# Performance work log

Measured on AMD Instinct MI355X. Metric: run time of the kernel, lower is better.

The kernel has to match this reference:

```python
import jax, jax.numpy as jnp
import numpy as np

# static config (matches init_kwargs)
C = 64            # dim_split = dim // 4
DIM = 256
HID = 128         # int(dim//4 * mlp_ratio), mlp_ratio=2
S = 64            # state_dim
NH, HD = 16, 4    # GA: num_heads = C // head_dim, head_dim = 4
AK, AP = 11, 5    # att_kernel, att_padding
B, H, W = 8, 28, 28


def conv2d(x, w, pad, stride=1, groups=1, bias=None):
    out = jax.lax.conv_general_dilated(
        x, w, (stride, stride), pad, feature_group_count=groups,
        dimension_numbers=('NCHW', 'OIHW', 'NCHW'))
    if bias is not None:
        out = out + bias[None, :, None, None]
    return out


def pw(x, w, b=None):  # 1x1 conv, w: (O, Cin)
    y = jnp.einsum('oc,bchw->bohw', w, x)
    return y if b is None else y + b[None, :, None, None]


def bn(x, p, eps=1e-5):  # eval-mode BatchNorm2d; p: (4, C) = gamma, beta, mean, var
    g, b, m, v = p
    s = g / jnp.sqrt(v + eps)
    return (x - m[None, :, None, None]) * s[None, :, None, None] + b[None, :, None, None]


def relu6(x):
    return jnp.minimum(jax.nn.relu(x), 6.0)


def maxpool3(x):  # 3x3, stride 1, pad 1
    return jax.lax.reduce_window(x, -jnp.inf, jax.lax.max, (1, 1, 3, 3), (1, 1, 1, 1),
                                 [(0, 0), (0, 0), (1, 1), (1, 1)])


def blurpool(x):  # antialiased_cnns.BlurPool(channels, stride=3), filt_size=4
    a = np.array([1.0, 3.0, 3.0, 1.0])
    filt = np.outer(a, a)
    filt = filt / filt.sum()
    c = x.shape[1]
    w = jnp.asarray(np.tile(filt[None, None], (c, 1, 1, 1)), x.dtype)
    xp = jnp.pad(x, ((0, 0), (0, 0), (1, 2), (1, 2)), mode='reflect')
    return conv2d(xp, w, [(0, 0), (0, 0)], stride=3, groups=c)


def h_transform(x):
    b, c, hs, ws = x.shape
    x = jnp.pad(x, ((0, 0), (0, 0), (0, 0), (0, ws))).reshape(b, c, -1)[..., :-ws]
    return x.reshape(b, c, hs, 2 * ws - 1)


def inv_h_transform(x):
    b, c, hs, _ = x.shape
    x = jnp.pad(x.reshape(b, c, -1), ((0, 0), (0, 0), (0, hs)))
    return x.reshape(b, c, hs, 2 * hs)[..., :hs]


def v_transform(x):
    return h_transform(x.transpose(0, 1, 3, 2)).transpose(0, 1, 3, 2)


def inv_v_transform(x):
    return inv_h_transform(x.transpose(0, 1, 3, 2)).transpose(0, 1, 3, 2)


def _forward(x, dw1_w, dw1_b, bn_dw1, f1_w, f1_b, f2_w, f2_b, g_w, g_b, bn_g,
             dw2_w, dw2_b, hatt1_w, vatt1_w, hatt2_w, vatt2_w, bn_mra,
             bcdt_w, ssd_dw_w, hz_w, out_w, A_param, D_param,
             qkv_w, proj_w, bn_norm4, mlp1_w, bn_mlp, mlp2_w, bn_norm1):
    shortcut = x
    x1, x2, x3, x4 = jnp.split(x, 4, axis=1)

    # --- branch 1: dwconv + star-gated MLP ---
    x1o = bn(conv2d(x1, dw1_w, [(3, 3), (3, 3)], groups=C, bias=dw1_b), bn_dw1)
    x1 = relu6(pw(x1o, f1_w, f1_b)) * pw(x1o, f2_w, f2_b)
    x1 = conv2d(bn(pw(x1, g_w, g_b), bn_g), dw2_w, [(3, 3), (3, 3)], groups=C, bias=dw2_b)

    # --- branch 2: MRA ---
    xt = blurpool(maxpool3(x2))  # (B, C, 10, 10)
    xh1 = conv2d(xt, hatt1_w, [(AP, AP), (1, 1)], groups=C)
    xw1 = conv2d(xt, vatt1_w, [(1, 1), (AP, AP)], groups=C)
    xh2 = inv_h_transform(conv2d(h_transform(xt), hatt2_w, [(AP, AP), (1, 1)], groups=C))
    xw2 = inv_v_transform(conv2d(v_transform(xt), vatt2_w, [(1, 1), (AP, AP)], groups=C))
    att = jax.nn.sigmoid(bn(xh1 + xw1 + xh2 + xw2, bn_mra))
    hs, ws = att.shape[-2], att.shape[-1]
    ri = (jnp.arange(H) * hs) // H  # nearest-neighbor upsampling indices
    ci = (jnp.arange(W) * ws) // W
    x2 = x2 * att[:, :, ri][:, :, :, ci]

    # --- branch 3: HSMSSD (hidden-state-mixer SSD) ---
    L = H * W
    xs = x3.reshape(B, C, L)
    bcdt = conv2d(jnp.einsum('oc,bcl->bol', bcdt_w, xs).reshape(B, 3 * S, H, W),
                  ssd_dw_w, [(1, 1), (1, 1)], groups=3 * S).reshape(B, 3 * S, L)
    Bm, Cm, dt = jnp.split(bcdt, 3, axis=1)              # each (B, S, L)
    A = jax.nn.softmax(dt + A_param[None, :, None], axis=-1)
    h = jnp.einsum('bcl,bsl->bcs', xs, A * Bm)           # (B, C, S)
    h_, z = jnp.split(jnp.einsum('oc,bcs->bos', hz_w, h), 2, axis=1)
    h_ = jnp.einsum('oc,bcs->bos', out_w, h_ * jax.nn.silu(z) + h_ * D_param)
    x3 = jnp.einsum('bcs,bsl->bcl', h_, Cm).reshape(B, C, H, W)

    # --- branch 4: GA full attention + BN residual (stage == 3) ---
    t = x4.reshape(B, C, L).transpose(0, 2, 1)           # (B, N, C)
    qkv = (t @ qkv_w.T).reshape(B, L, 3, NH, HD).transpose(2, 0, 3, 1, 4)
    q, k, v = qkv[0], qkv[1], qkv[2]
    attn = jax.nn.softmax(jnp.einsum('bhnd,bhmd->bhnm', q, k) * HD ** -0.5, axis=-1)
    o = jnp.einsum('bhnm,bhmd->bhnd', attn, v).transpose(0, 2, 1, 3).reshape(B, L, NH * HD)
    x4 = bn(x4 + (o @ proj_w.T).transpose(0, 2, 1).reshape(B, C, H, W), bn_norm4)

    # --- merge + MLP ---
    xa = jnp.concatenate([x1, x2, x3, x4], axis=1)
    m = pw(jax.nn.relu(bn(pw(xa, mlp1_w), bn_mlp)), mlp2_w)
    return shortcut + bn(m, bn_norm1)


def setup_inputs() -> dict:
    key = jax.random.key(0)
    ks = iter(jax.random.split(key, 64))

    def w(shape, s=0.05):
        return jax.random.normal(next(ks), shape, dtype=jnp.float32) * s

    def bnp(c):
        g = 1.0 + 0.1 * jax.random.normal(next(ks), (c,), dtype=jnp.float32)
        b = 0.1 * jax.random.normal(next(ks), (c,), dtype=jnp.float32)
        m = 0.1 * jax.random.normal(next(ks), (c,), dtype=jnp.float32)
        v = 0.5 + jax.random.uniform(next(ks), (c,), dtype=jnp.float32)
        return jnp.stack([g, b, m, v])

    return dict(
        x=jax.random.normal(next(ks), (B, DIM, H, W), dtype=jnp.float32),
        dw1_w=w((C, 1, 7, 7), 0.1), dw1_b=w((C,), 0.02), bn_dw1=bnp(C),
        f1_w=w((HID, C)), f1_b=w((HID,), 0.02),
        f2_w=w((HID, C)), f2_b=w((HID,), 0.02),
        g_w=w((C, HID)), g_b=w((C,), 0.02), bn_g=bnp(C),
        dw2_w=w((C, 1, 7, 7), 0.1), dw2_b=w((C,), 0.02),
        hatt1_w=w((C, 1, AK, 3), 0.1), vatt1_w=w((C, 1, 3, AK), 0.1),
        hatt2_w=w((C, 1, AK, 3), 0.1), vatt2_w=w((C, 1, 3, AK), 0.1),
        bn_mra=bnp(C),
        bcdt_w=w((3 * S, C)), ssd_dw_w=w((3 * S, 1, 3, 3), 0.1),
        hz_w=w((2 * C, C)), out_w=w((C, C)),
        A_param=jax.random.uniform(next(ks), (S,), dtype=jnp.float32, minval=1.0, maxval=16.0),
        D_param=jnp.ones((1,), dtype=jnp.float32),
        qkv_w=w((3 * NH * HD, C)), proj_w=w((C, NH * HD)),
        bn_norm4=bnp(C),
        mlp1_w=w((HID, DIM)), bn_mlp=bnp(HID), mlp2_w=w((DIM, HID)),
        bn_norm1=bnp(DIM),
    )


def reference(x, dw1_w, dw1_b, bn_dw1, f1_w, f1_b, f2_w, f2_b, g_w, g_b, bn_g,
              dw2_w, dw2_b, hatt1_w, vatt1_w, hatt2_w, vatt2_w, bn_mra,
              bcdt_w, ssd_dw_w, hz_w, out_w, A_param, D_param,
              qkv_w, proj_w, bn_norm4, mlp1_w, bn_mlp, mlp2_w, bn_norm1):
    return _forward(x, dw1_w, dw1_b, bn_dw1, f1_w, f1_b, f2_w, f2_b, g_w, g_b, bn_g,
                    dw2_w, dw2_b, hatt1_w, vatt1_w, hatt2_w, vatt2_w, bn_mra,
                    bcdt_w, ssd_dw_w, hz_w, out_w, A_param, D_param,
                    qkv_w, proj_w, bn_norm4, mlp1_w, bn_mlp, mlp2_w, bn_norm1)
```

## Files before the change

kernel.cpp:

```cpp
#include <hip/hip_runtime.h>
#include <hip/hip_bf16.h>
#include <math.h>

#define DEV __device__ __forceinline__

constexpr int B=8, C=64, DIM=256, HID=128, S=64, NH=16, HD=4, LPIX=784;
constexpr int NPIX = B*LPIX;
constexpr int CH   = (NPIX+255)/256;
constexpr int QB   = 12*((NPIX+511)/512);

constexpr size_t OFF_X1O = 0;
constexpr size_t OFF_T1  = OFF_X1O + (size_t)B*C*LPIX;
constexpr size_t OFF_T2  = OFF_T1  + (size_t)B*HID*LPIX;
constexpr size_t OFF_XA  = OFF_T2  + (size_t)B*C*LPIX;
constexpr size_t OFF_BC2 = OFF_XA  + (size_t)B*DIM*LPIX;
constexpr size_t OFF_WGT = OFF_BC2 + (size_t)B*192*LPIX;
constexpr size_t OFF_H   = OFF_WGT + (size_t)B*S*LPIX;
constexpr size_t OFF_HO  = OFF_H   + (size_t)4*B*C*S;
constexpr size_t OFF_QKV = OFF_HO  + (size_t)B*C*S;
constexpr size_t OFF_O   = OFF_QKV + (size_t)3*B*NH*LPIX*HD;
constexpr size_t OFF_LS  = OFF_O   + (size_t)4*B*LPIX*C;
constexpr size_t OFF_MID = OFF_LS  + (size_t)4*B*NH*LPIX;

DEV float bnorm(float x, const float* p, int c, int nc){
  float g=p[c], bb=p[nc+c], m=p[2*nc+c], v=p[3*nc+c];
  return (x-m)*(g*rsqrtf(v+1e-5f))+bb;
}
DEV int refl(int p){ int k=p-1; if(k<0)k=-k; if(k>27)k=54-k; return k; }

DEV bool upix(int blk, int tid, int ngroups, int& grp, int& b, int& l){
  grp = blk % ngroups;
  int gidx = (blk/ngroups)*256 + tid;
  if(gidx >= NPIX) return false;
  b = gidx / LPIX; l = gidx % LPIX;
  return true;
}

DEV void body_dw1t(int bc, int tid, float* xs, const float* X, const float* w, const float* bias, const float* bnp, float* out){
  int c = bc & 63, b = bc >> 6;
  const float* xp = X + ((size_t)(b*DIM+c))*LPIX;
  for(int i=tid;i<34*34;i+=256) xs[i]=0.f;
  __syncthreads();
  for(int i=tid;i<LPIX;i+=256){ int y=i/28, x=i%28; xs[(y+3)*34+(x+3)]=xp[i]; }
  __syncthreads();
  const float* wc = w + (size_t)c*49;
  float bs = bias[c];
  for(int i=tid;i<LPIX;i+=256){
    int y=i/28, x=i%28;
    float s = bs;
    #pragma unroll
    for(int ky=0;ky<7;ky++){
      #pragma unroll
      for(int kx=0;kx<7;kx++)
        s += xs[(y+ky)*34 + x+kx]*wc[ky*7+kx];
    }
    out[((size_t)(b*C+c))*LPIX + i] = bnorm(s,bnp,c,C);
  }
}

DEV void body_branch2(int bc, int tid, float* smem, const float* X,
                      const float* h1w,const float* v1w,const float* h2w,const float* v2w,
                      const float* bnp, float* xa){
  int c = bc & 63, b = bc >> 6;
  float* xs  = smem;
  float* mp  = smem+LPIX;
  float* xt  = smem+2*LPIX;
  float* attv= smem+2*LPIX+100;
  const float* xp = X + ((size_t)(b*DIM+64+c))*LPIX;
  for(int i=tid;i<LPIX;i+=256) xs[i]=xp[i];
  __syncthreads();
  for(int i=tid;i<LPIX;i+=256){
    int y=i/28, x=i%28;
    float m=-1e30f;
    for(int dy=-1;dy<=1;dy++){ int iy=y+dy; if(iy<0||iy>=28) continue;
      for(int dx=-1;dx<=1;dx++){ int ix=x+dx; if(ix<0||ix>=28) continue;
        m=fmaxf(m,xs[iy*28+ix]); } }
    mp[i]=m;
  }
  __syncthreads();
  if(tid<100){
    int ii=tid/10, j=tid%10;
    const float fw[4]={0.125f,0.375f,0.375f,0.125f};
    float s=0;
    for(int ky=0;ky<4;ky++){ int rr=refl(3*ii+ky);
      for(int kx=0;kx<4;kx++){ int cc=refl(3*j+kx);
        s += fw[ky]*fw[kx]*mp[rr*28+cc]; } }
    xt[tid]=s;
  }
  __syncthreads();
  if(tid<100){
    int r=tid/10, j=tid%10;
    float s=0;
    for(int kh=0;kh<11;kh++){ int a=r+kh-5; if(a<0||a>=10) continue;
      for(int kw=0;kw<3;kw++){ int b2=j+kw-1; if(b2<0||b2>=10) continue;
        s+=xt[a*10+b2]*h1w[(size_t)c*33+kh*3+kw]; } }
    for(int kh=0;kh<3;kh++){ int a=r+kh-1; if(a<0||a>=10) continue;
      for(int kw=0;kw<11;kw++){ int b2=j+kw-5; if(b2<0||b2>=10) continue;
        s+=xt[a*10+b2]*v1w[(size_t)c*33+kh*11+kw]; } }
    { int t=20*r+j; int r2=t/19, j2=t%19;
      for(int kh=0;kh<11;kh++){ int a=r2+kh-5; if(a<0||a>=10) continue;
        for(int kw=0;kw<3;kw++){ int b2=j2+kw-1; if(b2<0||b2>=19) continue;
          int i2=19*a+b2; int row=i2/20, col=i2%20;
          if(col<10) s+=xt[row*10+col]*h2w[(size_t)c*33+kh*3+kw]; } } }
    { int t=20*j+r; int p=t%19, q=t/19;
      for(int kh=0;kh<3;kh++){ int a=p+kh-1; if(a<0||a>=19) continue;
        for(int kw=0;kw<11;kw++){ int b2=q+kw-5; if(b2<0||b2>=10) continue;
          int i2=19*b2+a; int row=i2/20, col=i2%20;
          if(col<10) s+=xt[col*10+row]*v2w[(size_t)c*33+kh*11+kw]; } } }
    s = bnorm(s,bnp,c,C);
    attv[tid] = 1.f/(1.f+__expf(-s));
  }
  __syncthreads();
  float* dst = xa + ((size_t)(b*DIM+64+c))*LPIX;
  for(int i=tid;i<LPIX;i+=256){
    int y=i/28, x=i%28;
    float a = attv[((y*10)/28)*10 + (x*10)/28];
    dst[i] = xs[i]*a;
  }
}

DEV void body_qkv(int blk, int tid, const float* X, const float* w, float* qkvb){
  int og = blk % 12;
  int p0 = (blk/12)*512 + tid;
  if(p0 >= NPIX) return;
  int o0 = og*16;
  int b0 = p0/LPIX, l0 = p0%LPIX;
  int p1 = p0 + 256;
  bool has1 = p1 < NPIX;
  int b1 = has1 ? p1/LPIX : b0, l1 = has1 ? p1%LPIX : l0;
  const float* xp0 = X + ((size_t)(b0*DIM+192))*LPIX + l0;
  const float* xp1 = X + ((size_t)(b1*DIM+192))*LPIX + l1;
  float s0[16], s1[16];
  #pragma unroll
  for(int t=0;t<16;t++){ s0[t]=0.f; s1[t]=0.f; }
  for(int c=0;c<C;c+=4){
    float a0=xp0[(size_t)c*LPIX],     a1=xp0[(size_t)(c+1)*LPIX],
          a2=xp0[(size_t)(c+2)*LPIX], a3=xp0[(size_t)(c+3)*LPIX];
    float e0=xp1[(size_t)c*LPIX],     e1=xp1[(size_t)(c+1)*LPIX],
          e2=xp1[(size_t)(c+2)*LPIX], e3=xp1[(size_t)(c+3)*LPIX];
    #pragma unroll
    for(int t=0;t<16;t++){
      const float* wr = w + (size_t)(o0+t)*C + c;
      float w0=wr[0], w1=wr[1], w2=wr[2], w3=wr[3];
      s0[t] += w0*a0 + w1*a1 + w2*a2 + w3*a3;
      s1[t] += w0*e0 + w1*e1 + w2*e2 + w3*e3;
    }
  }
  int which=o0>>6, head0=(o0&63)>>2;
  #pragma unroll
  for(int t4=0;t4<4;t4++){
    float4* dst = (float4*)(qkvb + (size_t)which*B*NH*LPIX*HD + ((size_t)((b0*NH+head0+t4)*LPIX+l0))*HD);
    *dst = make_float4(s0[4*t4],s0[4*t4+1],s0[4*t4+2],s0[4*t4+3]);
  }
  if(has1){
    #pragma unroll
    for(int t4=0;t4<4;t4++){
      float4* dst = (float4*)(qkvb + (size_t)which*B*NH*LPIX*HD + ((size_t)((b1*NH+head0+t4)*LPIX+l1))*HD);
      *dst = make_float4(s1[4*t4],s1[4*t4+1],s1[4*t4+2],s1[4*t4+3]);
    }
  }
}

DEV void body_bcdtssd(int blk, int tid, float* smem, const float* X, const float* w, const float* dww,
                      float* bc2, float* wgt){
  int b = blk/48, og = blk%48; int o0=og*4;
  float* bc1s = smem;
  float* dts1 = smem + 4*LPIX;
  float* red  = smem + 5*LPIX;
  const float* xp = X + ((size_t)(b*DIM+128))*LPIX;
  {
    int l0=tid, l1=tid+256, l2=tid+512;
    float acc0[4]={0,0,0,0}, acc1[4]={0,0,0,0}, acc2[4]={0,0,0,0};
    for(int c=0;c<C;c+=4){
      float x00=xp[(size_t)c*LPIX+l0],     x01=xp[(size_t)(c+1)*LPIX+l0],
            x02=xp[(size_t)(c+2)*LPIX+l0], x03=xp[(size_t)(c+3)*LPIX+l0];
      float x10=xp[(size_t)c*LPIX+l1],     x11=xp[(size_t)(c+1)*LPIX+l1],
            x12=xp[(size_t)(c+2)*LPIX+l1], x13=xp[(size_t)(c+3)*LPIX+l1];
      float x20=xp[(size_t)c*LPIX+l2],     x21=xp[(size_t)(c+1)*LPIX+l2],
            x22=xp[(size_t)(c+2)*LPIX+l2], x23=xp[(size_t)(c+3)*LPIX+l2];
      #pragma unroll
      for(int t=0;t<4;t++){
        const float* wr = w + (size_t)(o0+t)*C + c;
        float w0=wr[0], w1=wr[1], w2=wr[2], w3=wr[3];
        acc0[t] += w0*x00 + w1*x01 + w2*x02 + w3*x03;
        acc1[t] += w0*x10 + w1*x11 + w2*x12 + w3*x13;
        acc2[t] += w0*x20 + w1*x21 + w2*x22 + w3*x23;
      }
    }
    #pragma unroll
    for(int t=0;t<4;t++){
      bc1s[t*LPIX+l0]=acc0[t];
      bc1s[t*LPIX+l1]=acc1[t];
      bc1s[t*LPIX+l2]=acc2[t];
    }
    if(tid<16){
      int l=768+tid;
      float a0=0,a1=0,a2=0,a3=0;
      for(int c=0;c<C;c+=4){
        float x0=xp[(size_t)c*LPIX+l],     x1=xp[(size_t)(c+1)*LPIX+l],
              x2=xp[(size_t)(c+2)*LPIX+l], x3=xp[(size_t)(c+3)*LPIX+l];
        const float* w0p = w + (size_t)(o0+0)*C + c;
        const float* w1p = w + (size_t)(o0+1)*C + c;
        const float* w2p = w + (size_t)(o0+2)*C + c;
        const float* w3p = w + (size_t)(o0+3)*C + c;
        a0 += w0p[0]*x0 + w0p[1]*x1 + w0p[2]*x2 + w0p[3]*x3;
        a1 += w1p[0]*x0 + w1p[1]*x1 + w1p[2]*x2 + w1p[3]*x3;
        a2 += w2p[0]*x0 + w2p[1]*x1 + w2p[2]*x2 + w2p[3]*x3;
        a3 += w3p[0]*x0 + w3p[1]*x1 + w3p[2]*x2 + w3p[3]*x3;
      }
      bc1s[0*LPIX+l]=a0; bc1s[1*LPIX+l]=a1; bc1s[2*LPIX+l]=a2; bc1s[3*LPIX+l]=a3;
    }
  }
  __syncthreads();
  if(og < 32){
    for(int i=tid;i<4*LPIX;i+=256){
      int oo=i/LPIX, l=i%LPIX; int y=l/28, x=l%28;
      const float* p = bc1s + oo*LPIX;
      const float* wk = dww + (size_t)(o0+oo)*9;
      float s=0;
      for(int ky=0;ky<3;ky++){ int iy=y+ky-1; if(iy<0||iy>=28) continue;
        for(int kx=0;kx<3;kx++){ int ix=x+kx-1; if(ix<0||ix>=28) continue;
          s += p[iy*28+ix]*wk[ky*3+kx]; } }
      bc2[((size_t)(b*192+o0+oo))*LPIX + l] = s;
    }
  } else {
    int wv = tid>>6, lane = tid&63;
    for(int oo=0;oo<4;oo++){
      const float* p = bc1s + oo*LPIX;
      const float* wk = dww + (size_t)(o0+oo)*9;
      float lmax=-1e30f;
      for(int i=tid;i<LPIX;i+=256){
        int y=i/28, x=i%28;
        float s=0;
        for(int ky=0;ky<3;ky++){ int iy=y+ky-1; if(iy<0||iy>=28) continue;
          for(int kx=0;kx<3;kx++){ int ix=x+kx-1; if(ix<0||ix>=28) continue;
            s += p[iy*28+ix]*wk[ky*3+kx]; } }
        dts1[i]=s;
        lmax=fmaxf(lmax,s);
      }
      for(int off=32;off;off>>=1) lmax=fmaxf(lmax,__shfl_xor(lmax,off));
      if(lane==0) red[wv]=lmax;
      __syncthreads();
      float bmax = fmaxf(fmaxf(red[0],red[1]),fmaxf(red[2],red[3]));
      float lsum=0;
      for(int i=tid;i<LPIX;i+=256){
        float e=__expf(dts1[i]-bmax);
        dts1[i]=e; lsum+=e;
      }
      for(int off=32;off;off>>=1) lsum += __shfl_xor(lsum,off);
      if(lane==0) red[4+wv]=lsum;
      __syncthreads();
      float inv = 1.f/(red[4]+red[5]+red[6]+red[7]);
      int s_ = o0-128+oo;
      float* wp = wgt + ((size_t)(b*S+s_))*LPIX;
      for(int i=tid;i<LPIX;i+=256) wp[i] = dts1[i]*inv;
      __syncthreads();
    }
  }
}

DEV void body_attn(int blk, int tid, float4* ks, float4* vs, const float* qkvb,
                   float* ob, float* lsb){
  int bh = blk >> 2, ms = blk & 3;
  int b = bh>>4, h = bh&15;
  const float4* q4 = (const float4*)(qkvb + (size_t)bh*LPIX*HD);
  const float4* k4 = (const float4*)(qkvb + (size_t)(B*NH + bh)*LPIX*HD) + ms*196;
  const float4* v4 = (const float4*)(qkvb + (size_t)(2*B*NH + bh)*LPIX*HD) + ms*196;
  for(int i=tid;i<196;i+=256){ ks[i]=k4[i]; vs[i]=v4[i]; }
  __syncthreads();
  const float SC = 0.5f*1.44269504f;
  float* obp = ob + (size_t)ms*B*LPIX*C;
  float* lsq = lsb + (size_t)ms*B*NH*LPIX + (size_t)bh*LPIX;

  float4 q[3];
  #pragma unroll
  for(int j=0;j<3;j++){
    float4 t = q4[tid + 256*j];
    q[j] = make_float4(t.x*SC, t.y*SC, t.z*SC, t.w*SC);
  }
  float l0[3]={0,0,0}, l1[3]={0,0,0};
  float ax0[3]={0,0,0}, ax1[3]={0,0,0};
  float ay0[3]={0,0,0}, ay1[3]={0,0,0};
  float az0[3]={0,0,0}, az1[3]={0,0,0};
  float aw0[3]={0,0,0}, aw1[3]={0,0,0};
  for(int m=0;m<196;m+=2){
    float4 k0=ks[m], k1=ks[m+1];
    float4 v0=vs[m], v1=vs[m+1];
    #pragma unroll
    for(int j=0;j<3;j++){
      float s0 = q[j].x*k0.x + q[j].y*k0.y + q[j].z*k0.z + q[j].w*k0.w;
      float s1 = q[j].x*k1.x + q[j].y*k1.y + q[j].z*k1.z + q[j].w*k1.w;
      float p0 = __builtin_amdgcn_exp2f(s0);
      float p1 = __builtin_amdgcn_exp2f(s1);
      l0[j]+=p0;        l1[j]+=p1;
      ax0[j]+=p0*v0.x;  ax1[j]+=p1*v1.x;
      ay0[j]+=p0*v0.y;  ay1[j]+=p1*v1.y;
      az0[j]+=p0*v0.z;  az1[j]+=p1*v1.z;
      aw0[j]+=p0*v0.w;  aw1[j]+=p1*v1.w;
    }
  }
  #pragma unroll
  for(int j=0;j<3;j++){
    int r = tid + 256*j;
    *(float4*)(obp + ((size_t)(b*LPIX+r))*C + h*4) =
        make_float4(ax0[j]+ax1[j], ay0[j]+ay1[j], az0[j]+az1[j], aw0[j]+aw1[j]);
    lsq[r] = l0[j]+l1[j];
  }
  if(tid < 16){
    int r = 768 + tid;
    float4 t = q4[r];
    float4 qq = make_float4(t.x*SC,t.y*SC,t.z*SC,t.w*SC);
    float ls=0; float4 a=make_float4(0,0,0,0);
    for(int m=0;m<196;m++){
      float4 kv=ks[m], vv=vs[m];
      float sc = qq.x*kv.x+qq.y*kv.y+qq.z*kv.z+qq.w*kv.w;
      float p = __builtin_amdgcn_exp2f(sc);
      ls+=p; a.x+=p*vv.x; a.y+=p*vv.y; a.z+=p*vv.z; a.w+=p*vv.w;
    }
    *(float4*)(obp + ((size_t)(b*LPIX+r))*C + h*4) = a;
    lsq[r] = ls;
  }
}

DEV void body_star(int blk, int tid, const float* x1o, const float* f1w,const float* f1b,const float* f2w,const float* f2b,float* t1){
  int jg, b, l; if(!upix(blk, tid, 32, jg, b, l)) return;
  int j0=jg*4;
  const float* xp = x1o + (size_t)b*C*LPIX + l;
  float a[4], g[4];
  for(int t=0;t<4;t++){ a[t]=f1b[j0+t]; g[t]=f2b[j0+t]; }
  for(int c=0;c<C;c++){
    float xv = xp[(size_t)c*LPIX];
    for(int t=0;t<4;t++){ a[t]+=f1w[(size_t)(j0+t)*C+c]*xv; g[t]+=f2w[(size_t)(j0+t)*C+c]*xv; }
  }
  for(int t=0;t<4;t++){
    float av = fminf(fmaxf(a[t],0.f),6.f);
    t1[((size_t)(b*HID+j0+t))*LPIX + l] = av*g[t];
  }
}

DEV void body_gproj(int blk, int tid, const float* t1, const float* gw,const float* gb,const float* bnp,float* t2){
  int cg, b, l; if(!upix(blk, tid, 4, cg, b, l)) return;
  int c0=cg*16;
  const float* tp = t1 + (size_t)b*HID*LPIX + l;
  float s[16];
  #pragma unroll
  for(int t=0;t<16;t++) s[t]=gb[c0+t];
  for(int j=0;j<HID;j++){
    float xv = tp[(size_t)j*LPIX];
    #pragma unroll
    for(int t=0;t<16;t++) s[t]+=gw[(size_t)(c0+t)*HID+j]*xv;
  }
  #pragma unroll
  for(int t=0;t<16;t++) t2[((size_t)(b*C+c0+t))*LPIX + l]=bnorm(s[t],bnp,c0+t,C);
}

DEV void body_x4(int blk, int tid, const float* X, const float* ob, const float* lsb,
                 const float* projw, const float* bnp, float* xa){
  int cg, b, l; if(!upix(blk, tid, 4, cg, b, l)) return;
  int c0=cg*16;
  const float* p0 = ob + ((size_t)(b*LPIX+l))*C;
  const float* p1 = p0 + (size_t)B*LPIX*C;
  const float* p2 = p1 + (size_t)B*LPIX*C;
  const float* p3 = p2 + (size_t)B*LPIX*C;
  float s[16];
  #pragma unroll
  for(int t=0;t<16;t++) s[t]=0.f;
  for(int h=0;h<NH;h++){
    size_t li = ((size_t)(b*NH+h))*LPIX + l;
    float lsum = lsb[li] + lsb[(size_t)B*NH*LPIX+li] + lsb[(size_t)2*B*NH*LPIX+li] + lsb[(size_t)3*B*NH*LPIX+li];
    float iv = 1.f/lsum;
    float4 q0=*(const float4*)(p0+h*4), q1=*(const float4*)(p1+h*4),
           q2=*(const float4*)(p2+h*4), q3=*(const float4*)(p3+h*4);
    float ov0=(q0.x+q1.x+q2.x+q3.x)*iv;
    float ov1=(q0.y+q1.y+q2.y+q3.y)*iv;
    float ov2=(q0.z+q1.z+q2.z+q3.z)*iv;
    float ov3=(q0.w+q1.w+q2.w+q3.w)*iv;
    const float* pw = projw + h*4;
    #pragma unroll
    for(int t=0;t<16;t++){
      const float* pr = pw + (size_t)(c0+t)*C;
      s[t] += pr[0]*ov0 + pr[1]*ov1 + pr[2]*ov2 + pr[3]*ov3;
    }
  }
  #pragma unroll
  for(int t=0;t<16;t++){
    float v = s[t] + X[((size_t)(b*DIM+192+c0+t))*LPIX + l];
    xa[((size_t)(b*DIM+192+c0+t))*LPIX + l] = bnorm(v,bnp,c0+t,C);
  }
}

DEV void body_h(int blk, int tid, float* smem, const float* X, const float* wgt, const float* bc2, float* hq){
  int b = blk >> 6, sub = blk & 63;
  int tile = sub >> 2, qq = sub & 3;
  int ct = (tile>>2)*16, st = (tile&3)*16;
  float (*Xs)[99] = (float(*)[99])smem;
  float (*Ws)[99] = (float(*)[99])(smem + 16*99);
  int tc = tid>>4, ts = tid&15;
  float acc=0;
  #pragma unroll
  for(int half=0;half<2;half++){
    int lb = qq*196 + half*98;
    for(int i=tid;i<16*98;i+=256){
      int r=i/98, col=i%98;
      Xs[r][col] = X[((size_t)(b*DIM+128+ct+r))*LPIX + lb + col];
      Ws[r][col] = wgt[((size_t)(b*S+st+r))*LPIX + lb + col]
                 * bc2[((size_t)(b*192+st+r))*LPIX + lb + col];
    }
    __syncthreads();
    #pragma unroll 7
    for(int l=0;l<98;l++) acc += Xs[tc][l]*Ws[ts][l];
    __syncthreads();
  }
  hq[(size_t)qq*B*C*S + ((size_t)(b*C+ct+tc))*S + st+ts] = acc;
}

DEV void body_dw2t(int bc, int tid, float* xs, const float* t2, const float* w, const float* bias, float* xa){
  int c = bc & 63, b = bc >> 6;
  const float* tp = t2 + ((size_t)(b*C+c))*LPIX;
  for(int i=tid;i<34*34;i+=256) xs[i]=0.f;
  __syncthreads();
  for(int i=tid;i<LPIX;i+=256){ int y=i/28, x=i%28; xs[(y+3)*34+(x+3)]=tp[i]; }
  __syncthreads();
  const float* wc = w + (size_t)c*49;
  float bs = bias[c];
  for(int i=tid;i<LPIX;i+=256){
    int y=i/28, x=i%28;
    float s = bs;
    #pragma unroll
    for(int ky=0;ky<7;ky++){
      #pragma unroll
      for(int kx=0;kx<7;kx++)
        s += xs[(y+ky)*34 + x+kx]*wc[ky*7+kx];
    }
    xa[((size_t)(b*DIM+c))*LPIX + i] = s;
  }
}

DEV void body_mixho(int blk, int tid, float* smem, const float* hq, const float* hzw,
                    const float* Dp, const float* outw, float* ho){
  int b = blk >> 3, st = (blk & 7) * 8;
  float (*hs2)[8] = (float(*)[8])smem;
  float (*g1s)[8] = (float(*)[8])(smem + C*8);
  for(int i=tid;i<C*8;i+=256){
    int k=i>>3, si=i&7;
    size_t off = ((size_t)(b*C+k))*S + st + si;
    hs2[k][si] = hq[off] + hq[(size_t)B*C*S+off] + hq[(size_t)2*B*C*S+off] + hq[(size_t)3*B*C*S+off];
  }
  __syncthreads();
  float D = Dp[0];
  for(int i=tid;i<C*8;i+=256){
    int c=i>>3, si=i&7;
    float hv=0, zv=0;
    for(int k=0;k<C;k++){ float x=hs2[k][si]; hv+=hzw[(size_t)c*C+k]*x; zv+=hzw[(size_t)(C+c)*C+k]*x; }
    float sil = zv/(1.f+__expf(-zv));
    g1s[c][si]=hv*sil+hv*D;
  }
  __syncthreads();
  for(int i=tid;i<C*8;i+=256){
    int c=i>>3, si=i&7;
    float acc=0;
    for(int k=0;k<C;k++) acc+=outw[(size_t)c*C+k]*g1s[k][si];
    ho[((size_t)(b*C+c))*S + st + si]=acc;
  }
}

DEV void body_x3(int blk, int tid, const float* ho, const float* bc2, float* xa){
  int cg, b, l; if(!upix(blk, tid, 16, cg, b, l)) return;
  int c0=cg*4;
  const float* hp = ho + (size_t)(b*C+c0)*S;
  const float* cm = bc2 + ((size_t)(b*192+64))*LPIX + l;
  float s[4]={0,0,0,0};
  for(int s_=0;s_<S;s_++){
    float cv = cm[(size_t)s_*LPIX];
    for(int t=0;t<4;t++) s[t] += hp[(size_t)t*S+s_]*cv;
  }
  for(int t=0;t<4;t++)
    xa[((size_t)(b*DIM+128+c0+t))*LPIX + l] = s[t];
}

__global__ void k_s1(const float* X,
                     const float* bcdt_w, const float* ssd_dw, float* bc2, float* wgt,
                     const float* h1w,const float* v1w,const float* h2w,const float* v2w,const float* bn_mra,
                     const float* qkv_w, float* qkvb,
                     const float* dw1_w,const float* dw1_b,const float* bn_dw1,
                     float* xa, float* x1o){
  __shared__ float smem[5*LPIX+8];
  int blk = blockIdx.x, tid = threadIdx.x;
  if(blk < 384)            body_bcdtssd(blk, tid, smem, X, bcdt_w, ssd_dw, bc2, wgt);
  else if(blk < 896)       body_branch2(blk-384, tid, smem, X, h1w,v1w,h2w,v2w, bn_mra, xa);
  else if(blk < 896+QB)    body_qkv(blk-896, tid, X, qkv_w, qkvb);
  else                     body_dw1t(blk-(896+QB), tid, smem, X, dw1_w, dw1_b, bn_dw1, x1o);
}

__global__ void k_s2(const float* qkvb, float* ob, float* lsb,
                     const float* x1o, const float* f1w,const float* f1b,const float* f2w,const float* f2b, float* t1,
                     const float* X, const float* wgt, const float* bc2, float* hq){
  __shared__ float4 smem4[792];
  float* smem = (float*)smem4;
  int blk = blockIdx.x, tid = threadIdx.x;
  if(blk < 512)            body_attn(blk, tid, smem4, smem4+196, qkvb, ob, lsb);
  else if(blk < 512+32*CH) body_star(blk-512, tid, x1o, f1w,f1b,f2w,f2b, t1);
  else                     body_h(blk-(512+32*CH), tid, smem, X, wgt, bc2, hq);
}

__global__ void k_s3(const float* t1, const float* gw,const float* gb,const float* bn_g, float* t2,
                     const float* X, const float* ob, const float* lsb,
                     const float* projw, const float* bn_n4, float* xa,
                     const float* hq, const float* hzw, const float* Dp, const float* outw, float* ho){
  __shared__ float smem[2*C*8];
  int blk = blockIdx.x, tid = threadIdx.x;
  if(blk < 64)           body_mixho(blk, tid, smem, hq, hzw, Dp, outw, ho);
  else if(blk < 64+4*CH) body_gproj(blk-64, tid, t1, gw, gb, bn_g, t2);
  else                   body_x4(blk-(64+4*CH), tid, X, ob, lsb, projw, bn_n4, xa);
}

__global__ void k_s4(const float* t2, const float* dw2_w, const float* dw2_b, float* xa,
                     const float* ho, const float* bc2){
  __shared__ float smem[34*34];
  int blk = blockIdx.x, tid = threadIdx.x;
  if(blk < 512) body_dw2t(blk, tid, smem, t2, dw2_w, dw2_b, xa);
  else          body_x3(blk-512, tid, ho, bc2, xa);
}

__global__ void k_mid(const float* xa, const float* m1w, const float* bnp, float* mid){
  int jg, b, l; if(!upix(blockIdx.x, threadIdx.x, 32, jg, b, l)) return;
  int j0=jg*4;
  const float* xp = xa + (size_t)b*DIM*LPIX + l;
  float s[4]={0,0,0,0};
  for(int c=0;c<DIM;c++){
    float xv=xp[(size_t)c*LPIX];
    for(int t=0;t<4;t++) s[t]+=m1w[(size_t)(j0+t)*DIM+c]*xv;
  }
  for(int t=0;t<4;t++)
    mid[((size_t)(b*HID+j0+t))*LPIX + l] = fmaxf(bnorm(s[t],bnp,j0+t,HID),0.f);
}

__global__ void k_out(const float* X, const float* mid, const float* m2w, const float* bnp, float* out){
  int cg, b, l; if(!upix(blockIdx.x, threadIdx.x, 32, cg, b, l)) return;
  int c0=cg*8;
  const float* mp_ = mid + (size_t)b*HID*LPIX + l;
  float s[8]={0,0,0,0,0,0,0,0};
  for(int j=0;j<HID;j++){
    float mv=mp_[(size_t)j*LPIX];
    for(int t=0;t<8;t++) s[t]+=m2w[(size_t)(c0+t)*HID+j]*mv;
  }
  for(int t=0;t<8;t++){
    size_t oi = ((size_t)(b*DIM+c0+t))*LPIX + l;
    out[oi] = bnorm(s[t],bnp,c0+t,DIM) + X[oi];
  }
}

extern "C" void kernel_launch(void* const* d_in, const int* in_sizes, int n_in,
                              void* d_out, int out_size, void* d_ws, size_t ws_size,
                              hipStream_t stream) {
  const float* X      = (const float*)d_in[0];
  const float* dw1_w  = (const float*)d_in[1];
  const float* dw1_b  = (const float*)d_in[2];
  const float* bn_dw1 = (const float*)d_in[3];
  const float* f1_w   = (const float*)d_in[4];
  const float* f1_b   = (const float*)d_in[5];
  const float* f2_w   = (const float*)d_in[6];
  const float* f2_b   = (const float*)d_in[7];
  const float* g_w    = (const float*)d_in[8];
  const float* g_b    = (const float*)d_in[9];
  const float* bn_g   = (const float*)d_in[10];
  const float* dw2_w  = (const float*)d_in[11];
  const float* dw2_b  = (const float*)d_in[12];
  const float* hatt1w = (const float*)d_in[13];
  const float* vatt1w = (const float*)d_in[14];
  const float* hatt2w = (const float*)d_in[15];
  const float* vatt2w = (const float*)d_in[16];
  const float* bn_mra = (const float*)d_in[17];
  const float* bcdt_w = (const float*)d_in[18];
  const float* ssd_dw = (const float*)d_in[19];
  const float* hz_w   = (const float*)d_in[20];
  const float* out_w  = (const float*)d_in[21];
  const float* D_p    = (const float*)d_in[23];
  const float* qkv_w  = (const float*)d_in[24];
  const float* proj_w = (const float*)d_in[25];
  const float* bn_n4  = (const float*)d_in[26];
  const float* mlp1_w = (const float*)d_in[27];
  const float* bn_mlp = (const float*)d_in[28];
  const float* mlp2_w = (const float*)d_in[29];
  const float* bn_n1  = (const float*)d_in[30];

  float* ws   = (float*)d_ws;
  float* x1o  = ws+OFF_X1O;  float* t1  = ws+OFF_T1;  float* t2  = ws+OFF_T2;
  float* xa   = ws+OFF_XA;   float* bc2 = ws+OFF_BC2; float* wgt = ws+OFF_WGT;
  float* hq   = ws+OFF_H;    float* ho  = ws+OFF_HO;  float* qkvb= ws+OFF_QKV;
  float* ob   = ws+OFF_O;    float* lsb = ws+OFF_LS;  float* mid = ws+OFF_MID;

  dim3 blk(256);

  k_s1 <<<dim3(896+QB+512),blk,0,stream>>>(X, bcdt_w, ssd_dw, bc2, wgt,
                                     hatt1w,vatt1w,hatt2w,vatt2w,bn_mra,
                                     qkv_w, qkvb, dw1_w,dw1_b,bn_dw1, xa, x1o);
  k_s2 <<<dim3(512+32*CH+512),blk,0,stream>>>(qkvb, ob, lsb,
                                     x1o, f1_w,f1_b,f2_w,f2_b, t1,
                                     X, wgt, bc2, hq);
  k_s3 <<<dim3(64+8*CH),blk,0,stream>>>(t1, g_w,g_b,bn_g, t2,
                                     X, ob, lsb, proj_w, bn_n4, xa,
                                     hq, hz_w, D_p, out_w, ho);
  k_s4 <<<dim3(512+16*CH),blk,0,stream>>>(t2, dw2_w, dw2_b, xa, ho, bc2);
  k_mid<<<dim3(32*CH),blk,0,stream>>>(xa,mlp1_w,bn_mlp,mid);
  k_out<<<dim3(32*CH),blk,0,stream>>>(X,mid,mlp2_w,bn_n1,(float*)d_out);
}
```

Measured before the change: 283.8 us.

## Split attention blocks in half, use SoA K/V in LDS, parallelize SSD softmax per wave

The attention body now uses twice as many blocks, each handling half the query rows with two queries per thread. K/V are stored in shared memory as structure-of-arrays and read as float2 pairs. The SSD dt softmax now computes all four channels' convolutions up front and runs one softmax per wavefront, in parallel and without block barriers, which also shrinks the k_s1 shared buffer. The aim is better occupancy and latency hiding, at the cost of more blocks and redundant K/V loads per block.

After: 291.8 us. 1.03x slower.

```diff
diff --git a/kernel.cpp b/kernel.cpp
--- a/kernel.cpp
+++ b/kernel.cpp
@@ -165,8 +165,6 @@
                       float* bc2, float* wgt){
   int b = blk/48, og = blk%48; int o0=og*4;
   float* bc1s = smem;
-  float* dts1 = smem + 4*LPIX;
-  float* red  = smem + 5*LPIX;
   const float* xp = X + ((size_t)(b*DIM+128))*LPIX;
   {
     int l0=tid, l1=tid+256, l2=tid+512;
@@ -224,101 +222,100 @@
       bc2[((size_t)(b*192+o0+oo))*LPIX + l] = s;
     }
   } else {
-    int wv = tid>>6, lane = tid&63;
-    for(int oo=0;oo<4;oo++){
-      const float* p = bc1s + oo*LPIX;
-      const float* wk = dww + (size_t)(o0+oo)*9;
-      float lmax=-1e30f;
-      for(int i=tid;i<LPIX;i+=256){
-        int y=i/28, x=i%28;
+    float cv[13];
+    #pragma unroll
+    for(int k=0;k<13;k++){
+      int i = tid + k*256;
+      if(i < 4*LPIX){
+        int oo=i/LPIX, l=i%LPIX; int y=l/28, x=l%28;
+        const float* p = bc1s + oo*LPIX;
+        const float* wk = dww + (size_t)(o0+oo)*9;
         float s=0;
         for(int ky=0;ky<3;ky++){ int iy=y+ky-1; if(iy<0||iy>=28) continue;
           for(int kx=0;kx<3;kx++){ int ix=x+kx-1; if(ix<0||ix>=28) continue;
             s += p[iy*28+ix]*wk[ky*3+kx]; } }
-        dts1[i]=s;
-        lmax=fmaxf(lmax,s);
+        cv[k]=s;
       }
-      for(int off=32;off;off>>=1) lmax=fmaxf(lmax,__shfl_xor(lmax,off));
-      if(lane==0) red[wv]=lmax;
-      __syncthreads();
-      float bmax = fmaxf(fmaxf(red[0],red[1]),fmaxf(red[2],red[3]));
-      float lsum=0;
-      for(int i=tid;i<LPIX;i+=256){
-        float e=__expf(dts1[i]-bmax);
-        dts1[i]=e; lsum+=e;
-      }
-      for(int off=32;off;off>>=1) lsum += __shfl_xor(lsum,off);
-      if(lane==0) red[4+wv]=lsum;
-      __syncthreads();
-      float inv = 1.f/(red[4]+red[5]+red[6]+red[7]);
-      int s_ = o0-128+oo;
-      float* wp = wgt + ((size_t)(b*S+s_))*LPIX;
-      for(int i=tid;i<LPIX;i+=256) wp[i] = dts1[i]*inv;
-      __syncthreads();
-    }
-  }
-}
-
-DEV void body_attn(int blk, int tid, float4* ks, float4* vs, const float* qkvb,
+    }
+    __syncthreads();
+    #pragma unroll
+    for(int k=0;k<13;k++){ int i=tid+k*256; if(i<4*LPIX) bc1s[i]=cv[k]; }
+    __syncthreads();
+    int wv = tid>>6, lane = tid&63;
+    float* row = bc1s + wv*LPIX;
+    float mx = -1e30f;
+    for(int l=lane;l<LPIX;l+=64) mx = fmaxf(mx, row[l]);
+    for(int off=32;off;off>>=1) mx = fmaxf(mx, __shfl_xor(mx,off));
+    float sum=0;
+    for(int l=lane;l<LPIX;l+=64){ float e=__expf(row[l]-mx); row[l]=e; sum+=e; }
+    for(int off=32;off;off>>=1) sum += __shfl_xor(sum,off);
+    float inv = 1.f/sum;
+    int s_ = o0-128+wv;
+    float* wp = wgt + ((size_t)(b*S+s_))*LPIX;
+    for(int l=lane;l<LPIX;l+=64) wp[l] = row[l]*inv;
+  }
+}
+
+DEV void body_attn(int blk, int tid, float* smem, const float* qkvb,
                    float* ob, float* lsb){
-  int bh = blk >> 2, ms = blk & 3;
+  int bh = blk >> 3, ms = (blk >> 1) & 3, half = blk & 1;
   int b = bh>>4, h = bh&15;
-  const float4* q4 = (const float4*)(qkvb + (size_t)bh*LPIX*HD);
+  float* kx = smem;        float* ky = smem+196;
+  float* kz = smem+392;    float* kw = smem+588;
+  float* vx = smem+784;    float* vy = smem+980;
+  float* vz = smem+1176;   float* vw = smem+1372;
   const float4* k4 = (const float4*)(qkvb + (size_t)(B*NH + bh)*LPIX*HD) + ms*196;
   const float4* v4 = (const float4*)(qkvb + (size_t)(2*B*NH + bh)*LPIX*HD) + ms*196;
-  for(int i=tid;i<196;i+=256){ ks[i]=k4[i]; vs[i]=v4[i]; }
-  __syncthreads();
+  for(int i=tid;i<196;i+=256){
+    float4 kv=k4[i]; kx[i]=kv.x; ky[i]=kv.y; kz[i]=kv.z; kw[i]=kv.w;
+    float4 vv=v4[i]; vx[i]=vv.x; vy[i]=vv.y; vz[i]=vv.z; vw[i]=vv.w;
+  }
   const float SC = 0.5f*1.44269504f;
+  const float4* q4 = (const float4*)(qkvb + (size_t)bh*LPIX*HD);
+  int rbase = half*392;
+  int r0 = rbase + tid;
+  int r1 = rbase + 256 + tid;
+  bool has1 = tid < 136;
+  float4 qa = q4[r0];
+  float4 qb = has1 ? q4[r1] : qa;
+  qa.x*=SC; qa.y*=SC; qa.z*=SC; qa.w*=SC;
+  qb.x*=SC; qb.y*=SC; qb.z*=SC; qb.w*=SC;
+  __syncthreads();
   float* obp = ob + (size_t)ms*B*LPIX*C;
   float* lsq = lsb + (size_t)ms*B*NH*LPIX + (size_t)bh*LPIX;
-
-  float4 q[3];
-  #pragma unroll
-  for(int j=0;j<3;j++){
-    float4 t = q4[tid + 256*j];
-    q[j] = make_float4(t.x*SC, t.y*SC, t.z*SC, t.w*SC);
-  }
-  float l0[3]={0,0,0}, l1[3]={0,0,0};
-  float ax0[3]={0,0,0}, ax1[3]={0,0,0};
-  float ay0[3]={0,0,0}, ay1[3]={0,0,0};
-  float az0[3]={0,0,0}, az1[3]={0,0,0};
-  float aw0[3]={0,0,0}, aw1[3]={0,0,0};
-  for(int m=0;m<196;m+=2){
-    float4 k0=ks[m], k1=ks[m+1];
-    float4 v0=vs[m], v1=vs[m+1];
-    #pragma unroll
-    for(int j=0;j<3;j++){
-      float s0 = q[j].x*k0.x + q[j].y*k0.y + q[j].z*k0.z + q[j].w*k0.w;
-      float s1 = q[j].x*k1.x + q[j].y*k1.y + q[j].z*k1.z + q[j].w*k1.w;
-      float p0 = __builtin_amdgcn_exp2f(s0);
-      float p1 = __builtin_amdgcn_exp2f(s1);
-      l0[j]+=p0;        l1[j]+=p1;
-      ax0[j]+=p0*v0.x;  ax1[j]+=p1*v1.x;
-      ay0[j]+=p0*v0.y;  ay1[j]+=p1*v1.y;
-      az0[j]+=p0*v0.z;  az1[j]+=p1*v1.z;
-      aw0[j]+=p0*v0.w;  aw1[j]+=p1*v1.w;
-    }
-  }
-  #pragma unroll
-  for(int j=0;j<3;j++){
-    int r = tid + 256*j;
-    *(float4*)(obp + ((size_t)(b*LPIX+r))*C + h*4) =
-        make_float4(ax0[j]+ax1[j], ay0[j]+ay1[j], az0[j]+az1[j], aw0[j]+aw1[j]);
-    lsq[r] = l0[j]+l1[j];
-  }
-  if(tid < 16){
-    int r = 768 + tid;
-    float4 t = q4[r];
-    float4 qq = make_float4(t.x*SC,t.y*SC,t.z*SC,t.w*SC);
-    float ls=0; float4 a=make_float4(0,0,0,0);
-    for(int m=0;m<196;m++){
-      float4 kv=ks[m], vv=vs[m];
-      float sc = qq.x*kv.x+qq.y*kv.y+qq.z*kv.z+qq.w*kv.w;
-      float p = __builtin_amdgcn_exp2f(sc);
-      ls+=p; a.x+=p*vv.x; a.y+=p*vv.y; a.z+=p*vv.z; a.w+=p*vv.w;
-    }
-    *(float4*)(obp + ((size_t)(b*LPIX+r))*C + h*4) = a;
-    lsq[r] = ls;
+  float l0x=0,l0y=0, a0xx=0,a0xy=0, a0yx=0,a0yy=0, a0zx=0,a0zy=0, a0wx=0,a0wy=0;
+  float l1x=0,l1y=0, a1xx=0,a1xy=0, a1yx=0,a1yy=0, a1zx=0,a1zy=0, a1wx=0,a1wy=0;
+  for(int m=0;m<98;m++){
+    float2 kX=*(const float2*)(kx+2*m), kY=*(const float2*)(ky+2*m),
+           kZ=*(const float2*)(kz+2*m), kW=*(const float2*)(kw+2*m);
+    float2 vX=*(const float2*)(vx+2*m), vY=*(const float2*)(vy+2*m),
+           vZ=*(const float2*)(vz+2*m), vW=*(const float2*)(vw+2*m);
+    float s0x = qa.x*kX.x + qa.y*kY.x + qa.z*kZ.x + qa.w*kW.x;
+    float s0y = qa.x*kX.y + qa.y*kY.y + qa.z*kZ.y + qa.w*kW.y;
+    float p0x = __builtin_amdgcn_exp2f(s0x);
+    float p0y = __builtin_amdgcn_exp2f(s0y);
+    l0x += p0x;        l0y += p0y;
+    a0xx += p0x*vX.x;  a0xy += p0y*vX.y;
+    a0yx += p0x*vY.x;  a0yy += p0y*vY.y;
+    a0zx += p0x*vZ.x;  a0zy += p0y*vZ.y;
+    a0wx += p0x*vW.x;  a0wy += p0y*vW.y;
+    float s1x = qb.x*kX.x + qb.y*kY.x + qb.z*kZ.x + qb.w*kW.x;
+    float s1y = qb.x*kX.y + qb.y*kY.y + qb.z*kZ.y + qb.w*kW.y;
+    float p1x = __builtin_amdgcn_exp2f(s1x);
+    float p1y = __builtin_amdgcn_exp2f(s1y);
+    l1x += p1x;        l1y += p1y;
+    a1xx += p1x*vX.x;  a1xy += p1y*vX.y;
+    a1yx += p1x*vY.x;  a1yy += p1y*vY.y;
+    a1zx += p1x*vZ.x;  a1zy += p1y*vZ.y;
+    a1wx += p1x*vW.x;  a1wy += p1y*vW.y;
+  }
+  *(float4*)(obp + ((size_t)(b*LPIX+r0))*C + h*4) =
+      make_float4(a0xx+a0xy, a0yx+a0yy, a0zx+a0zy, a0wx+a0wy);
+  lsq[r0] = l0x+l0y;
+  if(has1){
+    *(float4*)(obp + ((size_t)(b*LPIX+r1))*C + h*4) =
+        make_float4(a1xx+a1xy, a1yx+a1yy, a1zx+a1zy, a1wx+a1wy);
+    lsq[r1] = l1x+l1y;
   }
 }
 
@@ -484,7 +481,7 @@
                      const float* qkv_w, float* qkvb,
                      const float* dw1_w,const float* dw1_b,const float* bn_dw1,
                      float* xa, float* x1o){
-  __shared__ float smem[5*LPIX+8];
+  __shared__ float smem[4*LPIX];
   int blk = blockIdx.x, tid = threadIdx.x;
   if(blk < 384)            body_bcdtssd(blk, tid, smem, X, bcdt_w, ssd_dw, bc2, wgt);
   else if(blk < 896)       body_branch2(blk-384, tid, smem, X, h1w,v1w,h2w,v2w, bn_mra, xa);
@@ -495,12 +492,11 @@
 __global__ void k_s2(const float* qkvb, float* ob, float* lsb,
                      const float* x1o, const float* f1w,const float* f1b,const float* f2w,const float* f2b, float* t1,
                      const float* X, const float* wgt, const float* bc2, float* hq){
-  __shared__ float4 smem4[792];
-  float* smem = (float*)smem4;
+  __shared__ float smem[3168];
   int blk = blockIdx.x, tid = threadIdx.x;
-  if(blk < 512)            body_attn(blk, tid, smem4, smem4+196, qkvb, ob, lsb);
-  else if(blk < 512+32*CH) body_star(blk-512, tid, x1o, f1w,f1b,f2w,f2b, t1);
-  else                     body_h(blk-(512+32*CH), tid, smem, X, wgt, bc2, hq);
+  if(blk < 1024)            body_attn(blk, tid, smem, qkvb, ob, lsb);
+  else if(blk < 1024+32*CH) body_star(blk-1024, tid, x1o, f1w,f1b,f2w,f2b, t1);
+  else                      body_h(blk-(1024+32*CH), tid, smem, X, wgt, bc2, hq);
 }
 
 __global__ void k_s3(const float* t1, const float* gw,const float* gb,const float* bn_g, float* t2,
@@ -595,7 +591,7 @@
   k_s1 <<<dim3(896+QB+512),blk,0,stream>>>(X, bcdt_w, ssd_dw, bc2, wgt,
                                      hatt1w,vatt1w,hatt2w,vatt2w,bn_mra,
                                      qkv_w, qkvb, dw1_w,dw1_b,bn_dw1, xa, x1o);
-  k_s2 <<<dim3(512+32*CH+512),blk,0,stream>>>(qkvb, ob, lsb,
+  k_s2 <<<dim3(1024+32*CH+512),blk,0,stream>>>(qkvb, ob, lsb,
                                      x1o, f1_w,f1_b,f2_w,f2_b, t1,
                                      X, wgt, bc2, hq);
   k_s3 <<<dim3(64+8*CH),blk,0,stream>>>(t1, g_w,g_b,bn_g, t2,
```
